# Kernel tuning notes

Measured on AMD Instinct MI355X. Metric: run time of the kernel, lower is better.

The kernel has to match this reference:

```python
import jax, jax.numpy as jnp
import numpy as np

N = 128          # grid sidelength -> N*N control points
BATCH = 16384    # number of query points
K = 9            # hard-coded K-NN in the module


def get_mgrid(sidelen):
    # matches torch get_mgrid with meshgrid indexing 'ij', flattened to (-1, 2)
    t = jnp.linspace(-1.0, 1.0, sidelen)
    gx, gy = jnp.meshgrid(t, t, indexing="ij")
    return jnp.stack([gx, gy], axis=-1).reshape(-1, 2)


def cubic_conv(s):
    # piecewise cubic (Keys) kernel; note original leaves |s|==1 and |s|>=2 at 0
    a = jnp.abs(s)
    p1 = 1.5 * a**3 - 2.5 * a**2 + 1.0
    p2 = -0.5 * a**3 + 2.5 * a**2 - 4.0 * a + 2.0
    return jnp.where(a < 1.0, p1, jnp.where((a > 1.0) & (a < 2.0), p2, 0.0))


def setup_inputs() -> dict:
    key = jax.random.key(0)
    kx, kw = jax.random.split(key)
    # query points in [-1, 1]^2 like the control grid
    x = jax.random.uniform(kx, (BATCH, 2), dtype=jnp.float32, minval=-1.0, maxval=1.0)
    # learned weights (zeros in the module init; random here for a non-trivial baseline)
    weights = jax.random.normal(kw, (N * N, 1), dtype=jnp.float32)
    control_points = get_mgrid(N).astype(jnp.float32)  # (N*N, 2), non-trainable
    return {"x": x, "weights": weights, "control_points": control_points}


def reference(x, weights, control_points):
    # squared pairwise distances (B, M) via GEMM expansion; matches ((X_i-X_j)**2).sum(-1)
    x2 = jnp.sum(x * x, axis=-1, keepdims=True)                  # (B, 1)
    c2 = jnp.sum(control_points * control_points, axis=-1)       # (M,)
    D = x2 + c2[None, :] - 2.0 * (x @ control_points.T)          # (B, M)
    # argKmin -> top_k of negated distances
    _, idx = jax.lax.top_k(-D, K)                                # (B, K) int32
    neighbors = control_points[idx]                              # (B, K, 2)
    # h = ||x[0] - x[1]|| (data-dependent bandwidth, as in the module)
    h = jnp.linalg.norm(x[0] - x[1])
    s = jnp.linalg.norm(x[:, None, :] - neighbors, axis=-1) / h  # (B, K)
    conv_out = cubic_conv(s)                                     # (B, K)
    out = jnp.sum(weights[idx] * conv_out[..., None], axis=1)    # (B, 1)
    return (out, x)
```

## Files before the change

kernel.cpp:

```cpp
#include <hip/hip_runtime.h>

#define BATCH 16384
#define NGRID 128
#define K 9
#define W 5

__global__ __launch_bounds__(64) void spline_knn_kernel(
    const float* __restrict__ x,
    const float* __restrict__ wts,
    const float* __restrict__ cp,
    float* __restrict__ out)
{
    int b = blockIdx.x * 64 + threadIdx.x;

    float2 xv = ((const float2*)x)[b];
    float x0 = xv.x, x1 = xv.y;

    float e0 = __fadd_rn(x[0], -x[2]);
    float e1 = __fadd_rn(x[1], -x[3]);
    float h = sqrtf(__fadd_rn(__fmul_rn(e0, e0), __fmul_rn(e1, e1)));

    float x2s = __fadd_rn(__fmul_rn(x0, x0), __fmul_rn(x1, x1));

    float pr = (x0 + 1.0f) * 63.5f;
    float pc = (x1 + 1.0f) * 63.5f;
    int r0 = min(max((int)floorf(pr + 0.5f) - 2, 0), NGRID - W);
    int c0 = min(max((int)floorf(pc + 0.5f) - 2, 0), NGRID - W);

    float tr[W], tc[W];
#pragma unroll
    for (int i = 0; i < W; ++i) tr[i] = cp[2 * ((r0 + i) * NGRID)];
#pragma unroll
    for (int j = 0; j < W; ++j) tc[j] = cp[2 * (r0 * NGRID + c0 + j) + 1];

    float ar[W], br[W], ac[W];
#pragma unroll
    for (int i = 0; i < W; ++i) { ar[i] = __fmul_rn(tr[i], tr[i]); br[i] = __fmul_rn(x0, tr[i]); }
#pragma unroll
    for (int j = 0; j < W; ++j) { ac[j] = __fmul_rn(tc[j], tc[j]); }

    unsigned long long best[K];
#pragma unroll
    for (int i = 0; i < K; ++i) best[i] = ~0ULL;

#pragma unroll
    for (int i = 0; i < W; ++i) {
        int mrow = (r0 + i) * NGRID + c0;
#pragma unroll
        for (int j = 0; j < W; ++j) {
            float c2s = __fadd_rn(ar[i], ac[j]);
            float tmp = __fadd_rn(x2s, c2s);
            float dot = __fmaf_rn(x1, tc[j], br[i]);
            float D   = __fmaf_rn(-2.0f, dot, tmp);

            unsigned ub = __float_as_uint(D);
            ub ^= ((unsigned)((int)ub >> 31)) | 0x80000000u;
            unsigned long long key =
                ((unsigned long long)ub << 32) | (unsigned)(mrow + j);

#pragma unroll
            for (int q = 0; q < K; ++q) {
                bool lt = key < best[q];
                unsigned long long lo = lt ? key : best[q];
                unsigned long long hi = lt ? best[q] : key;
                best[q] = lo;
                key = hi;
            }
        }
    }

    float invh = 1.0f / h;
    float acc = 0.0f;
#pragma unroll
    for (int q = 0; q < K; ++q) {
        unsigned hi = (unsigned)(best[q] >> 32);
        int m = (int)(best[q] & 0xFFFFFFFFull);
        unsigned mask = ((unsigned)((int)(~hi) >> 31)) | 0x80000000u;
        float D = __uint_as_float(hi ^ mask);
        float s = sqrtf(fmaxf(D, 0.0f)) * invh;
        float a2 = s * s;
        float a3 = a2 * s;
        float conv;
        if (s < 1.0f)                    conv = 1.5f * a3 - 2.5f * a2 + 1.0f;
        else if (s > 1.0f && s < 2.0f)   conv = -0.5f * a3 + 2.5f * a2 - 4.0f * s + 2.0f;
        else                             conv = 0.0f;
        acc += wts[m] * conv;
    }

    out[b] = acc;
    ((float2*)(out + BATCH))[b] = xv;
}

extern "C" void kernel_launch(void* const* d_in, const int* in_sizes, int n_in,
                              void* d_out, int out_size, void* d_ws, size_t ws_size,
                              hipStream_t stream) {
    const float* x  = (const float*)d_in[0];
    const float* w  = (const float*)d_in[1];
    const float* cp = (const float*)d_in[2];
    float* out = (float*)d_out;

    spline_knn_kernel<<<BATCH / 64, 64, 0, stream>>>(x, w, cp, out);
}
```

Measured before the change: 61.16 us.

## Replace 64-bit insertion-sort top-K with pairwise rank counting over 5x5 window

Drops the sequential 64-bit compare-swap insertion network and instead computes all 25 window distances, ranks each by pairwise comparison counting, and masks weights to the 9 smallest. The 25 window weights are prefetched up front so the gathers no longer depend on the sort result, and the sum uses four partial accumulators. The aim is to remove the serial dependency chain and 64-bit selects, at the cost of 300 float compares, cubic evaluation for all 25 points, and extra registers. Ties are ordered by position, which should match the index tiebreak, but summation order differs from the reference.

```diff
diff --git a/kernel.cpp b/kernel.cpp
--- a/kernel.cpp
+++ b/kernel.cpp
@@ -27,6 +27,13 @@
     int r0 = min(max((int)floorf(pr + 0.5f) - 2, 0), NGRID - W);
     int c0 = min(max((int)floorf(pc + 0.5f) - 2, 0), NGRID - W);
 
+    float wv[W * W];
+#pragma unroll
+    for (int i = 0; i < W; ++i)
+#pragma unroll
+        for (int j = 0; j < W; ++j)
+            wv[W * i + j] = wts[(r0 + i) * NGRID + (c0 + j)];
+
     float tr[W], tc[W];
 #pragma unroll
     for (int i = 0; i < W; ++i) tr[i] = cp[2 * ((r0 + i) * NGRID)];
@@ -39,55 +46,50 @@
 #pragma unroll
     for (int j = 0; j < W; ++j) { ac[j] = __fmul_rn(tc[j], tc[j]); }
 
-    unsigned long long best[K];
-#pragma unroll
-    for (int i = 0; i < K; ++i) best[i] = ~0ULL;
-
+    float d[W * W];
 #pragma unroll
     for (int i = 0; i < W; ++i) {
-        int mrow = (r0 + i) * NGRID + c0;
 #pragma unroll
         for (int j = 0; j < W; ++j) {
             float c2s = __fadd_rn(ar[i], ac[j]);
             float tmp = __fadd_rn(x2s, c2s);
             float dot = __fmaf_rn(x1, tc[j], br[i]);
-            float D   = __fmaf_rn(-2.0f, dot, tmp);
-
-            unsigned ub = __float_as_uint(D);
-            ub ^= ((unsigned)((int)ub >> 31)) | 0x80000000u;
-            unsigned long long key =
-                ((unsigned long long)ub << 32) | (unsigned)(mrow + j);
-
-#pragma unroll
-            for (int q = 0; q < K; ++q) {
-                bool lt = key < best[q];
-                unsigned long long lo = lt ? key : best[q];
-                unsigned long long hi = lt ? best[q] : key;
-                best[q] = lo;
-                key = hi;
-            }
+            d[W * i + j] = __fmaf_rn(-2.0f, dot, tmp);
         }
     }
 
+    int rank[W * W];
+#pragma unroll
+    for (int i = 0; i < W * W; ++i) rank[i] = 0;
+#pragma unroll
+    for (int i = 0; i < W * W; ++i)
+#pragma unroll
+        for (int j = i + 1; j < W * W; ++j) {
+            int le = (d[i] <= d[j]) ? 1 : 0;
+            rank[j] += le;
+            rank[i] += le ^ 1;
+        }
+
     float invh = 1.0f / h;
-    float acc = 0.0f;
+    float acc0 = 0.0f, acc1 = 0.0f, acc2 = 0.0f, acc3 = 0.0f;
 #pragma unroll
-    for (int q = 0; q < K; ++q) {
-        unsigned hi = (unsigned)(best[q] >> 32);
-        int m = (int)(best[q] & 0xFFFFFFFFull);
-        unsigned mask = ((unsigned)((int)(~hi) >> 31)) | 0x80000000u;
-        float D = __uint_as_float(hi ^ mask);
-        float s = sqrtf(fmaxf(D, 0.0f)) * invh;
+    for (int q = 0; q < W * W; ++q) {
+        float s = sqrtf(fmaxf(d[q], 0.0f)) * invh;
         float a2 = s * s;
         float a3 = a2 * s;
         float conv;
         if (s < 1.0f)                    conv = 1.5f * a3 - 2.5f * a2 + 1.0f;
         else if (s > 1.0f && s < 2.0f)   conv = -0.5f * a3 + 2.5f * a2 - 4.0f * s + 2.0f;
         else                             conv = 0.0f;
-        acc += wts[m] * conv;
+        float wsel = (rank[q] < K) ? wv[q] : 0.0f;
+        float term = wsel * conv;
+        if      ((q & 3) == 0) acc0 += term;
+        else if ((q & 3) == 1) acc1 += term;
+        else if ((q & 3) == 2) acc2 += term;
+        else                   acc3 += term;
     }
 
-    out[b] = acc;
+    out[b] = (acc0 + acc1) + (acc2 + acc3);
     ((float2*)(out + BATCH))[b] = xv;
 }
 
```

New measurement: 63.54 us. 3.9% more time.
